# Performance work log

Measured on AMD Instinct MI355X. Metric: run time of the kernel, lower is better.

Reference implementation:

```python
import jax, jax.numpy as jnp
import numpy as np

S = 2048        # query length
P = 2048        # past (cached) length
E = 1024        # n_embd
H = 16          # n_head
D = E // H      # head dim
NEG = -10000.0  # module's m1e4 buffer


def setup_inputs() -> dict:
    key = jax.random.key(0)
    ks = jax.random.split(key, 6)
    x = jax.random.normal(ks[0], (S, E), dtype=jnp.float32)
    past_key = jax.random.normal(ks[1], (H, P, D), dtype=jnp.float32)
    past_value = jax.random.normal(ks[2], (H, P, D), dtype=jnp.float32)
    # causal mask over [q_len, kv_len]: query i attends to kv j <= i + P
    q_idx = jnp.arange(S)[:, None]
    k_idx = jnp.arange(P + S)[None, :]
    mask = (k_idx <= q_idx + P)[None, :, :]  # [1, S, P+S] bool
    c_attn_w = jax.random.normal(ks[3], (E, 3 * E), dtype=jnp.float32) * 0.02
    c_attn_b = jnp.zeros((3 * E,), dtype=jnp.float32)
    c_proj_w = jax.random.normal(ks[4], (E, E), dtype=jnp.float32) * 0.02
    c_proj_b = jnp.zeros((E,), dtype=jnp.float32)
    return {"x": x, "past_key": past_key, "past_value": past_value,
            "mask": mask, "c_attn_w": c_attn_w, "c_attn_b": c_attn_b,
            "c_proj_w": c_proj_w, "c_proj_b": c_proj_b}


def reference(x, past_key, past_value, mask, c_attn_w, c_attn_b, c_proj_w, c_proj_b):
    # c_attn: [S, E] @ [E, 3E] + b -> [S, 3, E]
    qkv = (x @ c_attn_w + c_attn_b).reshape(S, 3, E)
    q, k, v = qkv[:, 0], qkv[:, 1], qkv[:, 2]
    # split_heads: [S, E] -> [H, S, D]
    split = lambda t: t.reshape(S, H, D).transpose(1, 0, 2)
    q, k, v = split(q), split(k), split(v)
    # KV cache concat along seq
    k = jnp.concatenate([past_key, k], axis=1)    # [H, P+S, D]
    v = jnp.concatenate([past_value, v], axis=1)  # [H, P+S, D]
    present = jnp.stack([k, v])                   # [2, H, P+S, D]
    # attention with materialized scores (faithful to original)
    w = jnp.einsum('hqd,hkd->hqk', q, k) / jnp.sqrt(jnp.float32(D))
    w = jnp.where(mask, w, jnp.float32(NEG))
    w = jax.nn.softmax(w, axis=-1)
    a = jnp.einsum('hqk,hkd->hqd', w, v)          # [H, S, D]
    # merge_heads: [H, S, D] -> [S, E]
    a = a.transpose(1, 0, 2).reshape(S, E)
    a = a @ c_proj_w + c_proj_b
    return (a, present)
```

## Files before the change

kernel.cpp:

```cpp
#include <hip/hip_runtime.h>


#define SDIM 2048
#define PDIM 2048
#define TDIM 4096
#define EDIM 1024
#define HNUM 16
#define DDIM 64

typedef short bf16x8 __attribute__((ext_vector_type(8)));
typedef float f32x4 __attribute__((ext_vector_type(4)));
typedef unsigned int u32x2 __attribute__((ext_vector_type(2)));

__device__ __forceinline__ unsigned short f2bf(float f) {
    union { float f; unsigned u; } v; v.f = f;
    unsigned r = v.u + 0x7fffu + ((v.u >> 16) & 1u);
    return (unsigned short)(r >> 16);
}

__device__ __forceinline__ void async16(const void* g, void* l) {
    __builtin_amdgcn_global_load_lds(
        (const __attribute__((address_space(1))) void*)g,
        (__attribute__((address_space(3))) void*)l, 16, 0, 0);
}


__global__ __launch_bounds__(256) void k_cvt_x(const float* __restrict__ in,
                                               short* __restrict__ out) {
    int i = (blockIdx.x * 256 + threadIdx.x) * 4;
    f32x4 v = *(const f32x4*)(in + i);
    unsigned lo = f2bf(v[0]) | ((unsigned)f2bf(v[1]) << 16);
    unsigned hi = f2bf(v[2]) | ((unsigned)f2bf(v[3]) << 16);
    u32x2 p = {lo, hi};
    *(u32x2*)(out + i) = p;
}

__global__ __launch_bounds__(256) void k_tr_cvt(const float* __restrict__ in,
                                                short* __restrict__ out,
                                                int R, int C) {
    __shared__ float tile[32][33];
    int cb = blockIdx.x * 32, rb = blockIdx.y * 32;
    int c = threadIdx.x & 31, r0 = threadIdx.x >> 5;
#pragma unroll
    for (int i = 0; i < 4; ++i)
        tile[r0 + 8 * i][c] = in[(rb + r0 + 8 * i) * C + cb + c];
    __syncthreads();
#pragma unroll
    for (int i = 0; i < 4; ++i)
        out[(cb + r0 + 8 * i) * R + rb + c] = (short)f2bf(tile[c][r0 + 8 * i]);
}

__global__ __launch_bounds__(256) void k_past_key(const float* __restrict__ pk,
                                                  short* __restrict__ Kb,
                                                  float* __restrict__ pk_out) {
    int i = (blockIdx.x * 256 + threadIdx.x) * 4;
    int h = i >> 17;
    f32x4 v = *(const f32x4*)(pk + i);
    int dst = i + (h << 17);
    *(f32x4*)(pk_out + dst) = v;
    unsigned lo = f2bf(v[0]) | ((unsigned)f2bf(v[1]) << 16);
    unsigned hi = f2bf(v[2]) | ((unsigned)f2bf(v[3]) << 16);
    u32x2 p = {lo, hi};
    *(u32x2*)(Kb + dst) = p;
}

__global__ __launch_bounds__(256) void k_past_value(const float* __restrict__ pv,
                                                    short* __restrict__ Vt,
                                                    float* __restrict__ pv_out) {
    __shared__ float tile[32][33];
    int h = blockIdx.z;
    int tb = blockIdx.x * 32;
    int db = blockIdx.y * 32;
    int c = threadIdx.x & 31, r0 = threadIdx.x >> 5;
    const float* src = pv + (h << 17);
    float* dst = pv_out + (h << 18);
#pragma unroll
    for (int i = 0; i < 4; ++i) {
        int r = r0 + 8 * i;
        float v = src[(tb + r) * DDIM + db + c];
        tile[r][c] = v;
        dst[(tb + r) * DDIM + db + c] = v;
    }
    __syncthreads();
#pragma unroll
    for (int i = 0; i < 4; ++i) {
        int d = r0 + 8 * i;
        Vt[(h * DDIM + db + d) * TDIM + tb + c] = (short)f2bf(tile[c][d]);
    }
}


template <int MODE>
__global__ __launch_bounds__(256) void k_gemm(
    const short* __restrict__ A, const short* __restrict__ Bt,
    const float* __restrict__ bias, int K,
    short* __restrict__ q_ws, short* __restrict__ Kb, short* __restrict__ Vt,
    float* __restrict__ pk, float* __restrict__ pv,
    float* __restrict__ outF, int N) {
    __shared__ short As[128 * 32];
    __shared__ short Bs[128 * 32];
    const int tid = threadIdx.x;
    const int m0 = blockIdx.y * 128, n0 = blockIdx.x * 128;
    const int w = tid >> 6, lane = tid & 63;
    const int wm = w >> 1, wn = w & 1;
    const int l15 = lane & 15, g = lane >> 4;

    f32x4 zero = {0.f, 0.f, 0.f, 0.f};
    f32x4 acc[4][4];
#pragma unroll
    for (int i = 0; i < 4; ++i)
#pragma unroll
        for (int j = 0; j < 4; ++j) acc[i][j] = zero;

    const int arow = tid >> 2;
    const int acol = (tid & 3) << 3;
    const short* Ab  = A  + (m0 + arow) * K + acol;
    const short* Ab2 = A  + (m0 + 64 + arow) * K + acol;
    const short* Bb  = Bt + (n0 + arow) * K + acol;
    const short* Bb2 = Bt + (n0 + 64 + arow) * K + acol;
    short* lA  = &As[tid * 8];
    short* lA2 = &As[2048 + tid * 8];
    short* lB  = &Bs[tid * 8];
    short* lB2 = &Bs[2048 + tid * 8];

    const int aoff = (wm * 64 + l15) * 32 + g * 8;
    const int boff = (wn * 64 + l15) * 32 + g * 8;

    for (int kt = 0; kt < K; kt += 32) {
        async16(Ab + kt, lA);
        async16(Ab2 + kt, lA2);
        async16(Bb + kt, lB);
        async16(Bb2 + kt, lB2);
        __syncthreads();
        bf16x8 af[4], bfr[4];
#pragma unroll
        for (int f = 0; f < 4; ++f) af[f]  = *(const bf16x8*)&As[aoff + f * 512];
#pragma unroll
        for (int f = 0; f < 4; ++f) bfr[f] = *(const bf16x8*)&Bs[boff + f * 512];
#pragma unroll
        for (int i = 0; i < 4; ++i)
#pragma unroll
            for (int j = 0; j < 4; ++j)
                acc[i][j] = __builtin_amdgcn_mfma_f32_16x16x32_bf16(
                    af[i], bfr[j], acc[i][j], 0, 0, 0);
        __syncthreads();
    }

    if (MODE == 1) {
#pragma unroll
        for (int j = 0; j < 4; ++j) {
            int ncol = n0 + wn * 64 + j * 16 + l15;
            float b = bias[ncol];
#pragma unroll
            for (int i = 0; i < 4; ++i) {
                int mb = m0 + wm * 64 + i * 16 + g * 4;
#pragma unroll
                for (int r = 0; r < 4; ++r)
                    outF[(mb + r) * N + ncol] = acc[i][j][r] + b;
            }
        }
    } else {
        const int sec = n0 >> 10;
#pragma unroll
        for (int j = 0; j < 4; ++j) {
            int ncol = n0 + wn * 64 + j * 16 + l15;
            float b = bias[ncol];
            int h = (ncol >> 6) & 15;
            int d = ncol & 63;
#pragma unroll
            for (int i = 0; i < 4; ++i) {
                int mb = m0 + wm * 64 + i * 16 + g * 4;
#pragma unroll
                for (int r = 0; r < 4; ++r) {
                    int s = mb + r;
                    float val = acc[i][j][r] + b;
                    if (sec == 0) {
                        q_ws[(h * SDIM + s) * DDIM + d] = (short)f2bf(val * 0.125f);
                    } else if (sec == 1) {
                        int idx = (h * TDIM + PDIM + s) * DDIM + d;
                        pk[idx] = val;
                        Kb[idx] = (short)f2bf(val);
                    } else {
                        pv[(h * TDIM + PDIM + s) * DDIM + d] = val;
                        Vt[(h * DDIM + d) * TDIM + PDIM + s] = (short)f2bf(val);
                    }
                }
            }
        }
    }
}

__global__ __launch_bounds__(256) void k_attn(const short* __restrict__ q_ws,
                                              const short* __restrict__ Kb,
                                              const short* __restrict__ Vt,
                                              short* __restrict__ aout) {
    __shared__ short Ks[2][64 * 64];
    __shared__ short Vs[2][64 * 64];
    __shared__ short Pl[4][16][72];
    const int tid = threadIdx.x;
    const int w = tid >> 6, lane = tid & 63;
    const int l15 = lane & 15, g = lane >> 4;
    const int h = blockIdx.x & 15;
    const int j = blockIdx.x >> 4;
    const int qt = (j & 1) ? (31 - (j >> 1)) : (j >> 1);
    const int q = qt * 64 + w * 16 + l15;

    const short* qb = q_ws + (h * SDIM + q) * DDIM;
    bf16x8 bq0 = *(const bf16x8*)(qb + g * 8);
    bf16x8 bq1 = *(const bf16x8*)(qb + 32 + g * 8);

    const short* Kh = Kb + h * TDIM * DDIM;
    const short* Vh = Vt + h * DDIM * TDIM;

    f32x4 zero = {0.f, 0.f, 0.f, 0.f};
    f32x4 o[4] = {zero, zero, zero, zero};
    float m_run = -1e30f, l_run = 0.f;
    const int ntiles = 33 + qt;
    short* myP = &Pl[w][0][0];
    const int r7 = (l15 & 7) << 4;

    auto stage = [&](int buf, int t) {
        const int t0 = t * 64;
        const char* Kg = (const char*)(Kh + t0 * DDIM);
        const char* Vg = (const char*)(Vh + t0);
#pragma unroll
        for (int i = 0; i < 2; ++i) {
            int b = w * 1024 + i * 4096 + (lane << 4);
            int sb = b ^ (((b >> 7) & 7) << 4);
            async16(Kg + sb, (char*)&Ks[buf][0] + w * 1024 + i * 4096);
            int vrow = b >> 7;
            int vcol = (b & 127) ^ ((vrow & 7) << 4);
            async16(Vg + vrow * (TDIM * 2) + vcol,
                    (char*)&Vs[buf][0] + w * 1024 + i * 4096);
        }
    };

    int cur = 0;
    stage(0, 0);
    __syncthreads();

    for (int t = 0; t < ntiles; ++t) {
        const int t0 = t * 64;
        if (t + 1 < ntiles) stage(cur ^ 1, t + 1);

        const char* Kc = (const char*)&Ks[cur][0];
        const char* Vc = (const char*)&Vs[cur][0];

        f32x4 sc[4];
#pragma unroll
        for (int kb = 0; kb < 4; ++kb) {
            const char* kr = Kc + (kb * 16 + l15) * 128;
            bf16x8 ak0 = *(const bf16x8*)(kr + ((g * 16) ^ r7));
            bf16x8 ak1 = *(const bf16x8*)(kr + ((64 + g * 16) ^ r7));
            f32x4 c = zero;
            c = __builtin_amdgcn_mfma_f32_16x16x32_bf16(ak0, bq0, c, 0, 0, 0);
            c = __builtin_amdgcn_mfma_f32_16x16x32_bf16(ak1, bq1, c, 0, 0, 0);
            sc[kb] = c;
        }
        if (t == ntiles - 1) {
#pragma unroll
            for (int kb = 0; kb < 4; ++kb)
#pragma unroll
                for (int i = 0; i < 4; ++i)
                    if (t0 + kb * 16 + g * 4 + i > PDIM + q) sc[kb][i] = -1e30f;
        }
        float tmax = sc[0][0];
#pragma unroll
        for (int kb = 0; kb < 4; ++kb)
#pragma unroll
            for (int i = 0; i < 4; ++i) tmax = fmaxf(tmax, sc[kb][i]);
        tmax = fmaxf(tmax, __shfl_xor(tmax, 16));
        tmax = fmaxf(tmax, __shfl_xor(tmax, 32));
        float m_new = fmaxf(m_run, tmax);
        float scale = __expf(m_run - m_new);
        float psum = 0.f;
        unsigned pw[8];
#pragma unroll
        for (int kb = 0; kb < 4; ++kb) {
            float p0 = __expf(sc[kb][0] - m_new);
            float p1 = __expf(sc[kb][1] - m_new);
            float p2 = __expf(sc[kb][2] - m_new);
            float p3 = __expf(sc[kb][3] - m_new);
            psum += (p0 + p1) + (p2 + p3);
            asm("v_cvt_pk_bf16_f32 %0, %1, %2"
                : "=v"(pw[2 * kb]) : "v"(p0), "v"(p1));
            asm("v_cvt_pk_bf16_f32 %0, %1, %2"
                : "=v"(pw[2 * kb + 1]) : "v"(p2), "v"(p3));
        }
        psum += __shfl_xor(psum, 16);
        psum += __shfl_xor(psum, 32);
        l_run = l_run * scale + psum;
        m_run = m_new;
#pragma unroll
        for (int d = 0; d < 4; ++d) o[d] *= scale;
#pragma unroll
        for (int kb = 0; kb < 4; ++kb) {
            u32x2 pk2 = {pw[2 * kb], pw[2 * kb + 1]};
            *(u32x2*)(myP + l15 * 72 + kb * 16 + g * 4) = pk2;
        }
        asm volatile("s_waitcnt lgkmcnt(0)" ::: "memory");
        __builtin_amdgcn_sched_barrier(0);
        bf16x8 bp0 = *(const bf16x8*)(myP + l15 * 72 + g * 8);
        bf16x8 bp1 = *(const bf16x8*)(myP + l15 * 72 + 32 + g * 8);
#pragma unroll
        for (int d = 0; d < 4; ++d) {
            const char* vr = Vc + (d * 16 + l15) * 128;
            bf16x8 av0 = *(const bf16x8*)(vr + ((g * 16) ^ r7));
            bf16x8 av1 = *(const bf16x8*)(vr + ((64 + g * 16) ^ r7));
            o[d] = __builtin_amdgcn_mfma_f32_16x16x32_bf16(av0, bp0, o[d], 0, 0, 0);
            o[d] = __builtin_amdgcn_mfma_f32_16x16x32_bf16(av1, bp1, o[d], 0, 0, 0);
        }
        __syncthreads();
        cur ^= 1;
    }
    float inv = 1.0f / l_run;
#pragma unroll
    for (int d = 0; d < 4; ++d) {
        unsigned lo = f2bf(o[d][0] * inv) | ((unsigned)f2bf(o[d][1] * inv) << 16);
        unsigned hi = f2bf(o[d][2] * inv) | ((unsigned)f2bf(o[d][3] * inv) << 16);
        u32x2 pk2 = {lo, hi};
        *(u32x2*)(aout + q * EDIM + h * DDIM + d * 16 + g * 4) = pk2;
    }
}


extern "C" void kernel_launch(void* const* d_in, const int* in_sizes, int n_in,
                              void* d_out, int out_size, void* d_ws, size_t ws_size,
                              hipStream_t stream) {
    const float* x          = (const float*)d_in[0];
    const float* past_key   = (const float*)d_in[1];
    const float* past_value = (const float*)d_in[2];
    const float* c_attn_w   = (const float*)d_in[4];
    const float* c_attn_b   = (const float*)d_in[5];
    const float* c_proj_w   = (const float*)d_in[6];
    const float* c_proj_b   = (const float*)d_in[7];

    float* out_a  = (float*)d_out;
    float* pk_out = out_a + (size_t)SDIM * EDIM;
    float* pv_out = pk_out + (size_t)HNUM * TDIM * DDIM;

    char* ws = (char*)d_ws;
    short* xb     = (short*)(ws);
    short* wqkvt  = (short*)(ws + (4u  << 20));
    short* wprojt = (short*)(ws + (10u << 20));
    short* q_ws   = (short*)(ws + (12u << 20));
    short* Kb     = (short*)(ws + (16u << 20));
    short* Vt     = (short*)(ws + (24u << 20));
    short* aout   = (short*)(ws + (32u << 20));

    k_cvt_x<<<2048, 256, 0, stream>>>(x, xb);
    k_tr_cvt<<<dim3(96, 32), 256, 0, stream>>>(c_attn_w, wqkvt, EDIM, 3 * EDIM);
    k_tr_cvt<<<dim3(32, 32), 256, 0, stream>>>(c_proj_w, wprojt, EDIM, EDIM);
    k_past_key<<<2048, 256, 0, stream>>>(past_key, Kb, pk_out);
    k_past_value<<<dim3(64, 2, 16), 256, 0, stream>>>(past_value, Vt, pv_out);

    k_gemm<0><<<dim3(24, 16), 256, 0, stream>>>(
        xb, wqkvt, c_attn_b, EDIM, q_ws, Kb, Vt, pk_out, pv_out,
        (float*)nullptr, 3 * EDIM);

    k_attn<<<512, 256, 0, stream>>>(q_ws, Kb, Vt, aout);

    k_gemm<1><<<dim3(8, 16), 256, 0, stream>>>(
        aout, wprojt, c_proj_b, EDIM,
        (short*)nullptr, (short*)nullptr, (short*)nullptr,
        (float*)nullptr, (float*)nullptr, out_a, EDIM);
}
```

Measured before the change: 265.6 us.

## Double-buffer GEMM LDS staging, use exp2 softmax with lazy rescale, swizzle P tile

The GEMM gets two LDS buffers, so the async load of the next K-slice is issued before computing on the current one, and one barrier per iteration is dropped. In attention, Q is pre-scaled by log2(e)/sqrt(D) so softmax can use exp2f. The running-max rescale of O and l is skipped when no lane's max increased. The P staging buffer drops its padding in favour of an XOR swizzle, which shrinks LDS use. These changes add complexity, and correctness depends on the async loads being complete when the single barrier is reached.

```diff
diff --git a/kernel.cpp b/kernel.cpp
--- a/kernel.cpp
+++ b/kernel.cpp
@@ -90,6 +90,8 @@
 }
 
 
+#define QSCALE 0.1803368801f
+
 template <int MODE>
 __global__ __launch_bounds__(256) void k_gemm(
     const short* __restrict__ A, const short* __restrict__ Bt,
@@ -97,8 +99,8 @@
     short* __restrict__ q_ws, short* __restrict__ Kb, short* __restrict__ Vt,
     float* __restrict__ pk, float* __restrict__ pv,
     float* __restrict__ outF, int N) {
-    __shared__ short As[128 * 32];
-    __shared__ short Bs[128 * 32];
+    __shared__ short As[2][128 * 32];
+    __shared__ short Bs[2][128 * 32];
     const int tid = threadIdx.x;
     const int m0 = blockIdx.y * 128, n0 = blockIdx.x * 128;
     const int w = tid >> 6, lane = tid & 63;
@@ -118,25 +120,27 @@
     const short* Ab2 = A  + (m0 + 64 + arow) * K + acol;
     const short* Bb  = Bt + (n0 + arow) * K + acol;
     const short* Bb2 = Bt + (n0 + 64 + arow) * K + acol;
-    short* lA  = &As[tid * 8];
-    short* lA2 = &As[2048 + tid * 8];
-    short* lB  = &Bs[tid * 8];
-    short* lB2 = &Bs[2048 + tid * 8];
 
     const int aoff = (wm * 64 + l15) * 32 + g * 8;
     const int boff = (wn * 64 + l15) * 32 + g * 8;
 
+    auto stage = [&](int buf, int kt) {
+        async16(Ab + kt,  &As[buf][tid * 8]);
+        async16(Ab2 + kt, &As[buf][2048 + tid * 8]);
+        async16(Bb + kt,  &Bs[buf][tid * 8]);
+        async16(Bb2 + kt, &Bs[buf][2048 + tid * 8]);
+    };
+
+    stage(0, 0);
+    __syncthreads();
+    int cur = 0;
     for (int kt = 0; kt < K; kt += 32) {
-        async16(Ab + kt, lA);
-        async16(Ab2 + kt, lA2);
-        async16(Bb + kt, lB);
-        async16(Bb2 + kt, lB2);
-        __syncthreads();
+        if (kt + 32 < K) stage(cur ^ 1, kt + 32);
         bf16x8 af[4], bfr[4];
 #pragma unroll
-        for (int f = 0; f < 4; ++f) af[f]  = *(const bf16x8*)&As[aoff + f * 512];
-#pragma unroll
-        for (int f = 0; f < 4; ++f) bfr[f] = *(const bf16x8*)&Bs[boff + f * 512];
+        for (int f = 0; f < 4; ++f) af[f]  = *(const bf16x8*)&As[cur][aoff + f * 512];
+#pragma unroll
+        for (int f = 0; f < 4; ++f) bfr[f] = *(const bf16x8*)&Bs[cur][boff + f * 512];
 #pragma unroll
         for (int i = 0; i < 4; ++i)
 #pragma unroll
@@ -144,6 +148,7 @@
                 acc[i][j] = __builtin_amdgcn_mfma_f32_16x16x32_bf16(
                     af[i], bfr[j], acc[i][j], 0, 0, 0);
         __syncthreads();
+        cur ^= 1;
     }
 
     if (MODE == 1) {
@@ -175,7 +180,7 @@
                     int s = mb + r;
                     float val = acc[i][j][r] + b;
                     if (sec == 0) {
-                        q_ws[(h * SDIM + s) * DDIM + d] = (short)f2bf(val * 0.125f);
+                        q_ws[(h * SDIM + s) * DDIM + d] = (short)f2bf(val * QSCALE);
                     } else if (sec == 1) {
                         int idx = (h * TDIM + PDIM + s) * DDIM + d;
                         pk[idx] = val;
@@ -196,7 +201,7 @@
                                               short* __restrict__ aout) {
     __shared__ short Ks[2][64 * 64];
     __shared__ short Vs[2][64 * 64];
-    __shared__ short Pl[4][16][72];
+    __shared__ short Pl[4][16][64];
     const int tid = threadIdx.x;
     const int w = tid >> 6, lane = tid & 63;
     const int l15 = lane & 15, g = lane >> 4;
@@ -216,8 +221,9 @@
     f32x4 o[4] = {zero, zero, zero, zero};
     float m_run = -1e30f, l_run = 0.f;
     const int ntiles = 33 + qt;
-    short* myP = &Pl[w][0][0];
-    const int r7 = (l15 & 7) << 4;
+    char* myP = (char*)&Pl[w][0][0];
+    const int pswz = (l15 & 7) << 4;
+    const int r7 = pswz;
 
     auto stage = [&](int buf, int t) {
         const int t0 = t * 64;
@@ -264,23 +270,29 @@
                 for (int i = 0; i < 4; ++i)
                     if (t0 + kb * 16 + g * 4 + i > PDIM + q) sc[kb][i] = -1e30f;
         }
-        float tmax = sc[0][0];
-#pragma unroll
-        for (int kb = 0; kb < 4; ++kb)
-#pragma unroll
-            for (int i = 0; i < 4; ++i) tmax = fmaxf(tmax, sc[kb][i]);
+        float t01 = fmaxf(fmaxf(sc[0][0], sc[0][1]), fmaxf(sc[0][2], sc[0][3]));
+        float t23 = fmaxf(fmaxf(sc[1][0], sc[1][1]), fmaxf(sc[1][2], sc[1][3]));
+        float t45 = fmaxf(fmaxf(sc[2][0], sc[2][1]), fmaxf(sc[2][2], sc[2][3]));
+        float t67 = fmaxf(fmaxf(sc[3][0], sc[3][1]), fmaxf(sc[3][2], sc[3][3]));
+        float tmax = fmaxf(fmaxf(t01, t23), fmaxf(t45, t67));
         tmax = fmaxf(tmax, __shfl_xor(tmax, 16));
         tmax = fmaxf(tmax, __shfl_xor(tmax, 32));
-        float m_new = fmaxf(m_run, tmax);
-        float scale = __expf(m_run - m_new);
+        if (!__all(tmax <= m_run)) {
+            float m_new = fmaxf(m_run, tmax);
+            float scale = exp2f(m_run - m_new);
+            l_run *= scale;
+#pragma unroll
+            for (int d = 0; d < 4; ++d) o[d] *= scale;
+            m_run = m_new;
+        }
         float psum = 0.f;
         unsigned pw[8];
 #pragma unroll
         for (int kb = 0; kb < 4; ++kb) {
-            float p0 = __expf(sc[kb][0] - m_new);
-            float p1 = __expf(sc[kb][1] - m_new);
-            float p2 = __expf(sc[kb][2] - m_new);
-            float p3 = __expf(sc[kb][3] - m_new);
+            float p0 = exp2f(sc[kb][0] - m_run);
+            float p1 = exp2f(sc[kb][1] - m_run);
+            float p2 = exp2f(sc[kb][2] - m_run);
+            float p3 = exp2f(sc[kb][3] - m_run);
             psum += (p0 + p1) + (p2 + p3);
             asm("v_cvt_pk_bf16_f32 %0, %1, %2"
                 : "=v"(pw[2 * kb]) : "v"(p0), "v"(p1));
@@ -289,19 +301,16 @@
         }
         psum += __shfl_xor(psum, 16);
         psum += __shfl_xor(psum, 32);
-        l_run = l_run * scale + psum;
-        m_run = m_new;
-#pragma unroll
-        for (int d = 0; d < 4; ++d) o[d] *= scale;
+        l_run += psum;
 #pragma unroll
         for (int kb = 0; kb < 4; ++kb) {
             u32x2 pk2 = {pw[2 * kb], pw[2 * kb + 1]};
-            *(u32x2*)(myP + l15 * 72 + kb * 16 + g * 4) = pk2;
+            *(u32x2*)(myP + l15 * 128 + ((kb * 32 + g * 8) ^ pswz)) = pk2;
         }
         asm volatile("s_waitcnt lgkmcnt(0)" ::: "memory");
         __builtin_amdgcn_sched_barrier(0);
-        bf16x8 bp0 = *(const bf16x8*)(myP + l15 * 72 + g * 8);
-        bf16x8 bp1 = *(const bf16x8*)(myP + l15 * 72 + 32 + g * 8);
+        bf16x8 bp0 = *(const bf16x8*)(myP + l15 * 128 + ((g * 16) ^ pswz));
+        bf16x8 bp1 = *(const bf16x8*)(myP + l15 * 128 + ((64 + g * 16) ^ pswz));
 #pragma unroll
         for (int d = 0; d < 4; ++d) {
             const char* vr = Vc + (d * 16 + l15) * 128;
```

After: 272.5 us. 2.6% more time.
